# Performance work log

Hardware: AMD Instinct MI355X
Metric: run time of the kernel (lower is better)

The kernel has to match this reference:

```python
import jax, jax.numpy as jnp
import numpy as np

H, P, G, NS, K = 8, 64, 64, 64, 3          # heads, dim_head, slice_num, d_state, d_conv
D_INNER = H * P                            # 512
CONV_DIM = D_INNER + 2 * NS                # 640
D_IN_PROJ = 2 * D_INNER + 2 * NS + 2 * H   # 1168


def setup_inputs() -> dict:
    key = jax.random.key(0)
    ks = jax.random.split(key, 10)
    dim, Bsz, N = 256, 4, 8192
    s = 0.02
    return {
        "x": jax.random.normal(ks[0], (Bsz, N, dim), jnp.float32),
        "W_fx": jax.random.normal(ks[1], (D_INNER, dim), jnp.float32) * s,
        "b_fx": jnp.zeros((D_INNER,), jnp.float32),
        "W_x": jax.random.normal(ks[2], (D_INNER, dim), jnp.float32) * s,
        "b_x": jnp.zeros((D_INNER,), jnp.float32),
        "W_slice": jax.random.normal(ks[3], (G, P), jnp.float32) * s,
        "b_slice": jnp.zeros((G,), jnp.float32),
        "temperature": jnp.full((1, H, 1, 1), 0.5, jnp.float32),
        "hy_in_w": jax.random.normal(ks[4], (D_IN_PROJ, D_INNER), jnp.float32) * s,
        "hy_conv_w": jax.random.normal(ks[5], (CONV_DIM, K), jnp.float32) * s,
        "hy_conv_b": jnp.zeros((CONV_DIM,), jnp.float32),
        "hy_dt_bias": jnp.log(jnp.expm1(jnp.full((H,), 0.01, jnp.float32))),
        "hy_A_log": jnp.log(jnp.linspace(1.0, 16.0, H)).astype(jnp.float32),
        "hy_D": jnp.ones((H,), jnp.float32),
        "hy_fcD_w": jax.random.normal(ks[6], (H, D_INNER), jnp.float32) * s,
        "hy_norm_w": jnp.ones((D_INNER,), jnp.float32),
        "hy_out_w": jax.random.normal(ks[7], (D_INNER, D_INNER), jnp.float32) * s,
        "out_w": jax.random.normal(ks[8], (dim, D_INNER), jnp.float32) * s,
        "out_b": jnp.zeros((dim,), jnp.float32),
    }


def _hydra(u, in_w, conv_w, conv_b, dt_bias, A_log, Dp, fcD_w, norm_w, out_w):
    # Bidirectional Mamba2-style selective scan (Hydra, non mem-eff path).
    Bt, L, _ = u.shape
    zxbcdt = u @ in_w.T                                   # (B, L, 1168)
    z = zxbcdt[..., :D_INNER]
    xBC = zxbcdt[..., D_INNER:D_INNER + CONV_DIM]
    dt = zxbcdt[..., -2 * H:]
    # fwd dts for fwd copies, time-flipped bwd dts stacked along batch
    dt = jnp.concatenate([dt[..., :H], jnp.flip(dt[..., H:], axis=1)], axis=0)
    dt = jax.nn.softplus(dt + dt_bias)                    # (2B, L, H)
    # depthwise causal conv, kernel K, left pad K-1 then silu
    xp = jnp.pad(xBC, ((0, 0), (K - 1, 0), (0, 0)))
    xBC = sum(xp[:, k:k + L, :] * conv_w[:, k] for k in range(K)) + conv_b
    xBC = jax.nn.silu(xBC)
    x = xBC[..., :D_INNER]
    Bm = xBC[..., D_INNER:D_INNER + NS]
    Cm = xBC[..., D_INNER + NS:]
    x_og = x
    x2 = jnp.concatenate([x, jnp.flip(x, 1)], 0).reshape(2 * Bt, L, H, P)
    B2 = jnp.concatenate([Bm, jnp.flip(Bm, 1)], 0)        # (2B, L, NS)
    C2 = jnp.concatenate([Cm, jnp.flip(Cm, 1)], 0)
    dA = jnp.exp(dt * (-jnp.exp(A_log)))                  # (2B, L, H)
    dBx = jnp.einsum('blh,bln,blhp->blhpn', dt, B2, x2)   # (2B, L, H, P, NS)

    def step(h, inp):
        dA_t, dBx_t, C_t = inp
        h = h * dA_t[:, :, None, None] + dBx_t
        return h, jnp.einsum('bhpn,bn->bhp', h, C_t)

    h0 = jnp.zeros((2 * Bt, H, P, NS), u.dtype)
    _, ys = jax.lax.scan(step, h0, (dA.transpose(1, 0, 2), dBx.transpose(1, 0, 2, 3, 4), C2.transpose(1, 0, 2)))
    y = ys.transpose(1, 0, 2, 3).reshape(2 * Bt, L, D_INNER)
    y_fw, y_bw = y[:Bt], jnp.flip(y[Bt:], 1)
    # quasiseparable: strictly-lower (shift fwd) + strictly-upper (shift bwd) + diagonal
    y = jnp.pad(y_fw[:, :-1], ((0, 0), (1, 0), (0, 0))) + jnp.pad(y_bw[:, 1:], ((0, 0), (0, 1), (0, 0)))
    y = y + x_og * jnp.repeat(x_og @ fcD_w.T + Dp, P, axis=-1)
    # gated RMSNorm (gate before norm), then out projection
    yg = y * jax.nn.silu(z)
    yg = yg * jax.lax.rsqrt(jnp.mean(jnp.square(yg), -1, keepdims=True) + 1e-5) * norm_w
    return yg @ out_w.T


def reference(x, W_fx, b_fx, W_x, b_x, W_slice, b_slice, temperature,
              hy_in_w, hy_conv_w, hy_conv_b, hy_dt_bias, hy_A_log, hy_D,
              hy_fcD_w, hy_norm_w, hy_out_w, out_w, out_b):
    B, N, _ = x.shape
    fx = (x @ W_fx.T + b_fx).reshape(B, N, H, P).transpose(0, 2, 1, 3)   # (B,H,N,P)
    xm = (x @ W_x.T + b_x).reshape(B, N, H, P).transpose(0, 2, 1, 3)
    temp = jnp.maximum(temperature, 1e-6)
    sw = jax.nn.softmax((xm @ W_slice.T + b_slice) / temp, axis=-1)      # (B,H,N,G)
    snorm = sw.sum(2)                                                     # (B,H,G)
    st = jnp.einsum('bhnc,bhng->bhgc', fx, sw) / (snorm + 1e-5)[..., None]
    st = st.transpose(0, 2, 1, 3).reshape(B, G, D_INNER)                  # (B,G,512)
    ot = _hydra(st, hy_in_w, hy_conv_w, hy_conv_b, hy_dt_bias, hy_A_log, hy_D,
                hy_fcD_w, hy_norm_w, hy_out_w)
    ot = ot.reshape(B, G, H, P).transpose(0, 2, 1, 3)                     # (B,H,G,P)
    out = jnp.einsum('bhgc,bhng->bhnc', ot, sw).transpose(0, 2, 1, 3).reshape(B, N, D_INNER)
    return out @ out_w.T + out_b
```

## Files before the change

kernel.cpp:

```cpp
#include <hip/hip_runtime.h>
#include <hip/hip_bf16.h>
#include <cstdint>
#include <cstddef>

#define Hh 8
#define DIN 512
#define CONVD 640
#define DPROJ 1168
#define NTOK 8192
#define DIM 256

typedef __attribute__((ext_vector_type(8))) short short8;
typedef __attribute__((ext_vector_type(4))) float f32x4;

static __device__ __forceinline__ float sigmoidf_(float x) { return 1.f / (1.f + expf(-x)); }
static __device__ __forceinline__ unsigned short f2b(float f) {
  __hip_bfloat16 h = __float2bfloat16(f);
  return *(unsigned short*)&h;
}
static __device__ __forceinline__ float b2f(unsigned short u) {
  union { unsigned int i; float f; } cv; cv.i = ((unsigned int)u) << 16; return cv.f;
}

__global__ __launch_bounds__(256) void k_cvt(
    const float* __restrict__ x, const float* __restrict__ wfx, const float* __restrict__ wx,
    const float* __restrict__ outw, const float* __restrict__ inw, const float* __restrict__ how,
    const float* __restrict__ bfx, const float* __restrict__ bx,
    unsigned short* __restrict__ xb, unsigned short* __restrict__ wcat,
    unsigned short* __restrict__ outwb, unsigned short* __restrict__ inwb,
    unsigned short* __restrict__ howb, float* __restrict__ bcat) {
  const int e = (blockIdx.x * 256 + threadIdx.x) * 4;
  if (e >= 9641984) {
    const int i = e - 9641984;
    float4 v;
    if (i < 512) v = *(const float4*)(bfx + i);
    else         v = *(const float4*)(bx + (i - 512));
    *(float4*)(bcat + i) = v;
    return;
  }
  const float* src; unsigned short* dst; int i;
  if (e < 8388608)       { i = e;           src = x;    dst = xb; }
  else if (e < 8519680)  { i = e - 8388608; src = wfx;  dst = wcat; }
  else if (e < 8650752)  { i = e - 8519680; src = wx;   dst = wcat + 131072; }
  else if (e < 8781824)  { i = e - 8650752; src = outw; dst = outwb; }
  else if (e < 9379840)  { i = e - 8781824; src = inw;  dst = inwb; }
  else                   { i = e - 9379840; src = how;  dst = howb; }
  float4 v = *(const float4*)(src + i);
  ushort4 o;
  o.x = f2b(v.x); o.y = f2b(v.y); o.z = f2b(v.z); o.w = f2b(v.w);
  *(ushort4*)(dst + i) = o;
}

__global__ __launch_bounds__(256) void k_fxxm(
    const unsigned short* __restrict__ xb, const unsigned short* __restrict__ wcat,
    const float* __restrict__ bcat, unsigned short* __restrict__ cb) {
  __shared__ unsigned short lds[17408];
  unsigned short* As = lds;
  unsigned short* Bs = lds + 8320;
  const int tid = threadIdx.x;
  const int m0 = blockIdx.x * 128;
  const int n0 = blockIdx.y * 128;
  const int w = tid >> 6, lane = tid & 63;
  const int l15 = lane & 15, kq = lane >> 4;
  const int wm = (w & 1) * 64, wn = (w >> 1) * 64;
  float bs[4];
#pragma unroll
  for (int j = 0; j < 4; ++j) bs[j] = bcat[n0 + wn + j * 16 + l15];
  f32x4 acc[4][4];
#pragma unroll
  for (int i = 0; i < 4; ++i)
#pragma unroll
    for (int j = 0; j < 4; ++j) acc[i][j] = (f32x4){0.f, 0.f, 0.f, 0.f};
  for (int kt = 0; kt < 256; kt += 64) {
#pragma unroll
    for (int i = 0; i < 4; ++i) {
      const int c = tid + 256 * i, m = c >> 3, kb = c & 7;
      *(short8*)&As[(kb * 130 + m) * 8] = *(const short8*)&xb[(size_t)(m0 + m) * 256 + kt + kb * 8];
      *(short8*)&Bs[(kb * 130 + m) * 8] = *(const short8*)&wcat[(size_t)(n0 + m) * 256 + kt + kb * 8];
    }
    __syncthreads();
#pragma unroll
    for (int kw = 0; kw < 2; ++kw) {
      short8 af[4], bfr[4];
#pragma unroll
      for (int i = 0; i < 4; ++i) {
        af[i]  = *(const short8*)&As[((kw * 4 + kq) * 130 + wm + i * 16 + l15) * 8];
        bfr[i] = *(const short8*)&Bs[((kw * 4 + kq) * 130 + wn + i * 16 + l15) * 8];
      }
#pragma unroll
      for (int i = 0; i < 4; ++i)
#pragma unroll
        for (int j = 0; j < 4; ++j)
          acc[i][j] = __builtin_amdgcn_mfma_f32_16x16x32_bf16(af[i], bfr[j], acc[i][j], 0, 0, 0);
    }
    __syncthreads();
  }
  unsigned short* Cs = lds;
#pragma unroll
  for (int i = 0; i < 4; ++i)
#pragma unroll
    for (int j = 0; j < 4; ++j)
#pragma unroll
      for (int r = 0; r < 4; ++r) {
        const int m = wm + i * 16 + kq * 4 + r;
        const int n = wn + j * 16 + l15;
        Cs[m * 136 + n] = f2b(acc[i][j][r] + bs[j]);
      }
  __syncthreads();
#pragma unroll
  for (int it = 0; it < 8; ++it) {
    const int c = tid + 256 * it;
    const int m = c >> 4, seg = c & 15;
    *(short8*)&cb[(size_t)(m0 + m) * 1024 + n0 + seg * 8] = *(const short8*)&Cs[m * 136 + seg * 8];
  }
}

__global__ __launch_bounds__(256) void k_sw(
    const unsigned short* __restrict__ cb, const float* __restrict__ Wslice,
    const float* __restrict__ bslice, const float* __restrict__ temperature,
    unsigned short* __restrict__ swb) {
  __shared__ unsigned short s_sw[256][72];
  const int tid = threadIdx.x;
  const int bh = blockIdx.y;
  const int b = bh >> 3, h = bh & 7;
  const int n0 = blockIdx.x * 256;
  const int w = tid >> 6, lane = tid & 63;
  const int l15 = lane & 15, kq = lane >> 4;
  const float invt = 1.f / fmaxf(temperature[h], 1e-6f);
  short8 bfr[2][4];
#pragma unroll
  for (int kt = 0; kt < 2; ++kt)
#pragma unroll
    for (int j = 0; j < 4; ++j) {
      const float* wp = Wslice + (j * 16 + l15) * 64 + kt * 32 + kq * 8;
      short8 t;
#pragma unroll
      for (int u = 0; u < 8; ++u) t[u] = (short)f2b(wp[u]);
      bfr[kt][j] = t;
    }
  float bs[4];
#pragma unroll
  for (int j = 0; j < 4; ++j) bs[j] = bslice[j * 16 + l15];
  f32x4 acc[4][4];
#pragma unroll
  for (int i = 0; i < 4; ++i)
#pragma unroll
    for (int j = 0; j < 4; ++j) acc[i][j] = (f32x4){0.f, 0.f, 0.f, 0.f};
#pragma unroll
  for (int kt = 0; kt < 2; ++kt) {
    short8 af[4];
#pragma unroll
    for (int i = 0; i < 4; ++i)
      af[i] = *(const short8*)&cb[((size_t)(b * NTOK) + n0 + w * 64 + i * 16 + l15) * 1024 +
                                  512 + h * 64 + kt * 32 + kq * 8];
#pragma unroll
    for (int i = 0; i < 4; ++i)
#pragma unroll
      for (int j = 0; j < 4; ++j)
        acc[i][j] = __builtin_amdgcn_mfma_f32_16x16x32_bf16(af[i], bfr[kt][j], acc[i][j], 0, 0, 0);
  }
#pragma unroll
  for (int i = 0; i < 4; ++i)
#pragma unroll
    for (int r = 0; r < 4; ++r) {
      float v[4];
      float m = -1e30f;
#pragma unroll
      for (int j = 0; j < 4; ++j) { v[j] = (acc[i][j][r] + bs[j]) * invt; m = fmaxf(m, v[j]); }
#pragma unroll
      for (int off = 8; off; off >>= 1) m = fmaxf(m, __shfl_xor(m, off));
      float s = 0.f;
#pragma unroll
      for (int j = 0; j < 4; ++j) { v[j] = expf(v[j] - m); s += v[j]; }
#pragma unroll
      for (int off = 8; off; off >>= 1) s += __shfl_xor(s, off);
      const float inv = 1.f / s;
      const int row = w * 64 + i * 16 + kq * 4 + r;
#pragma unroll
      for (int j = 0; j < 4; ++j) s_sw[row][j * 16 + l15] = f2b(v[j] * inv);
    }
  __syncthreads();
#pragma unroll
  for (int it = 0; it < 8; ++it) {
    const int c = tid + 256 * it;
    const int row = c >> 3, seg = c & 7;
    *(short8*)&swb[((size_t)bh * NTOK + n0 + row) * 64 + seg * 8] =
        *(const short8*)&s_sw[row][seg * 8];
  }
}

__global__ __launch_bounds__(256) void k_st(
    const unsigned short* __restrict__ swb, const unsigned short* __restrict__ cb,
    float* __restrict__ st_raw, float* __restrict__ snorm) {
  __shared__ unsigned short swT[64][136];
  __shared__ unsigned short fxT[64][136];
  const int tid = threadIdx.x;
  const int bh = blockIdx.y;
  const int b = bh >> 3, h = bh & 7;
  const int nbase = blockIdx.x * 512;
  const int w = tid >> 6, lane = tid & 63;
  const int l15 = lane & 15, kq = lane >> 4;
  f32x4 acc[4];
#pragma unroll
  for (int i = 0; i < 4; ++i) acc[i] = (f32x4){0.f, 0.f, 0.f, 0.f};
  float sn = 0.f;
  for (int nc = 0; nc < 4; ++nc) {
    const int n0 = nbase + nc * 128;
#pragma unroll
    for (int i = 0; i < 4; ++i) {
      const int c = tid + 256 * i, n = c >> 3, gc = c & 7;
      short8 sv = *(const short8*)&swb[((size_t)bh * NTOK + n0 + n) * 64 + gc * 8];
      short8 fv = *(const short8*)&cb[((size_t)(b * NTOK) + n0 + n) * 1024 + h * 64 + gc * 8];
#pragma unroll
      for (int u = 0; u < 8; ++u) {
        swT[gc * 8 + u][n] = (unsigned short)sv[u];
        fxT[gc * 8 + u][n] = (unsigned short)fv[u];
      }
    }
    __syncthreads();
    {
      const int g = tid & 63, q = tid >> 6;
#pragma unroll
      for (int nn = 0; nn < 32; ++nn) sn += b2f(swT[g][q * 32 + nn]);
    }
#pragma unroll
    for (int kw = 0; kw < 4; ++kw) {
      short8 bfr = *(const short8*)&fxT[w * 16 + l15][kw * 32 + kq * 8];
#pragma unroll
      for (int mi = 0; mi < 4; ++mi) {
        short8 af = *(const short8*)&swT[mi * 16 + l15][kw * 32 + kq * 8];
        acc[mi] = __builtin_amdgcn_mfma_f32_16x16x32_bf16(af, bfr, acc[mi], 0, 0, 0);
      }
    }
    __syncthreads();
  }
  float* stp = st_raw + (size_t)bh * 4096;
#pragma unroll
  for (int mi = 0; mi < 4; ++mi)
#pragma unroll
    for (int r = 0; r < 4; ++r)
      atomicAdd(&stp[(mi * 16 + kq * 4 + r) * 64 + w * 16 + l15], acc[mi][r]);
  atomicAdd(&snorm[bh * 64 + (tid & 63)], sn);
}

__global__ __launch_bounds__(256) void k_stnorm(
    const float* __restrict__ st_raw, const float* __restrict__ snorm,
    unsigned short* __restrict__ st2b) {
  const int idx = blockIdx.x * 256 + threadIdx.x;
  const int p = idx & 63, g = (idx >> 6) & 63, h = (idx >> 12) & 7, b = idx >> 15;
  const float v = st_raw[idx] / (snorm[(b * Hh + h) * 64 + g] + 1e-5f);
  st2b[(size_t)(b * 64 + g) * DIN + h * 64 + p] = f2b(v);
}

__global__ __launch_bounds__(256) void k_inproj(
    const unsigned short* __restrict__ st2b, const unsigned short* __restrict__ inwb,
    float* __restrict__ zx) {
  const int tid = threadIdx.x;
  const int m0 = blockIdx.x * 64;
  const int n0 = blockIdx.y * 64;
  const int w = tid >> 6, lane = tid & 63;
  const int l15 = lane & 15, kq = lane >> 4;
  f32x4 acc[4];
#pragma unroll
  for (int j = 0; j < 4; ++j) acc[j] = (f32x4){0.f, 0.f, 0.f, 0.f};
  const int arow = m0 + w * 16 + l15;
#pragma unroll
  for (int kc = 0; kc < 16; ++kc) {
    const short8 af = *(const short8*)&st2b[(size_t)arow * DIN + kc * 32 + kq * 8];
#pragma unroll
    for (int j = 0; j < 4; ++j) {
      int brow = n0 + j * 16 + l15;
      if (brow >= DPROJ) brow = 0;
      const short8 bfr = *(const short8*)&inwb[(size_t)brow * DIN + kc * 32 + kq * 8];
      acc[j] = __builtin_amdgcn_mfma_f32_16x16x32_bf16(af, bfr, acc[j], 0, 0, 0);
    }
  }
#pragma unroll
  for (int j = 0; j < 4; ++j)
#pragma unroll
    for (int r = 0; r < 4; ++r) {
      const int m = m0 + w * 16 + kq * 4 + r;
      const int c = n0 + j * 16 + l15;
      if (c < DPROJ) zx[(size_t)m * DPROJ + c] = acc[j][r];
    }
}

__global__ __launch_bounds__(256) void k_prep(
    const float* __restrict__ zx, const float* __restrict__ convw, const float* __restrict__ convb,
    const float* __restrict__ dtbias, const float* __restrict__ Alog,
    float* __restrict__ xbc, float* __restrict__ dt2, float* __restrict__ ldA2) {
  const int idx = blockIdx.x * 256 + threadIdx.x;
  const int NCONV = 4 * 64 * CONVD;
  if (idx < NCONV) {
    const int c = idx % CONVD;
    const int l = (idx / CONVD) & 63;
    const int b = idx / (CONVD * 64);
    float acc = convb[c];
#pragma unroll
    for (int k = 0; k < 3; ++k) {
      const int ls = l - 2 + k;
      if (ls >= 0) acc += zx[(size_t)(b * 64 + ls) * DPROJ + DIN + c] * convw[c * 3 + k];
    }
    xbc[idx] = acc * sigmoidf_(acc);
  } else if (idx < NCONV + 8 * 64 * 8) {
    const int j = idx - NCONV;
    const int h = j & 7, l = (j >> 3) & 63, bb = j >> 9;
    float raw;
    if (bb < 4) raw = zx[(size_t)(bb * 64 + l) * DPROJ + 1152 + h];
    else        raw = zx[(size_t)((bb - 4) * 64 + (63 - l)) * DPROJ + 1160 + h];
    const float d = raw + dtbias[h];
    const float sp = (d > 20.f) ? d : log1pf(expf(d));
    dt2[j] = sp;
    ldA2[j] = sp * -expf(Alog[h]);
  }
}

__global__ __launch_bounds__(256) void k_ssm(
    const float* __restrict__ xbc, const float* __restrict__ dt2, const float* __restrict__ ldA2,
    float* __restrict__ ys) {
  __shared__ unsigned short s_C[64][72];
  __shared__ unsigned short s_Bm[64][72];
  __shared__ unsigned short s_X[64][72];
  __shared__ unsigned short s_G[64][72];
  __shared__ float s_L[64];
  __shared__ float s_dt[64];
  const int blk = blockIdx.x;
  const int h = blk & 7, bb = blk >> 3;
  const int b = (bb < 4) ? bb : bb - 4;
  const bool rev = bb >= 4;
  const int tid = threadIdx.x;
  const int w = tid >> 6, lane = tid & 63;
  const int l15 = lane & 15, kq = lane >> 4;
  {
    const int l = tid >> 2, part = tid & 3;
    const int t = rev ? 63 - l : l;
    const float* src = xbc + (size_t)(b * 64 + l) * CONVD + DIN + part * 32;
#pragma unroll
    for (int u = 0; u < 32; u += 4) {
      float4 v = *(const float4*)(src + u);
      const int c = part * 32 + u;
      unsigned short* dst = (c < 64) ? &s_Bm[t][c] : &s_C[t][c - 64];
      dst[0] = f2b(v.x); dst[1] = f2b(v.y); dst[2] = f2b(v.z); dst[3] = f2b(v.w);
    }
    const float* xs = xbc + (size_t)(b * 64 + l) * CONVD + h * 64 + part * 16;
#pragma unroll
    for (int u = 0; u < 16; u += 4) {
      float4 v = *(const float4*)(xs + u);
      const int p = part * 16 + u;
      s_X[p + 0][t] = f2b(v.x); s_X[p + 1][t] = f2b(v.y);
      s_X[p + 2][t] = f2b(v.z); s_X[p + 3][t] = f2b(v.w);
    }
  }
  if (w == 0) {
    const float dtv = dt2[(bb * 64 + lane) * 8 + h];
    float ld = ldA2[(bb * 64 + lane) * 8 + h];
#pragma unroll
    for (int off = 1; off < 64; off <<= 1) {
      const float o = __shfl_up(ld, off);
      if (lane >= off) ld += o;
    }
    s_L[lane] = ld;
    s_dt[lane] = dtv;
  }
  __syncthreads();
  f32x4 accS[4];
#pragma unroll
  for (int i = 0; i < 4; ++i) accS[i] = (f32x4){0.f, 0.f, 0.f, 0.f};
#pragma unroll
  for (int kw = 0; kw < 2; ++kw) {
    const short8 bfr = *(const short8*)&s_Bm[w * 16 + l15][kw * 32 + kq * 8];
#pragma unroll
    for (int i = 0; i < 4; ++i) {
      const short8 af = *(const short8*)&s_C[i * 16 + l15][kw * 32 + kq * 8];
      accS[i] = __builtin_amdgcn_mfma_f32_16x16x32_bf16(af, bfr, accS[i], 0, 0, 0);
    }
  }
  const int s_idx = w * 16 + l15;
  const float Ls = s_L[s_idx];
  const float dts = s_dt[s_idx];
#pragma unroll
  for (int i = 0; i < 4; ++i)
#pragma unroll
    for (int r = 0; r < 4; ++r) {
      const int t = i * 16 + kq * 4 + r;
      const float g = (s_idx <= t) ? accS[i][r] * expf(s_L[t] - Ls) * dts : 0.f;
      s_G[t][s_idx] = f2b(g);
    }
  __syncthreads();
  f32x4 accY[4];
#pragma unroll
  for (int i = 0; i < 4; ++i) accY[i] = (f32x4){0.f, 0.f, 0.f, 0.f};
#pragma unroll
  for (int kw = 0; kw < 2; ++kw) {
    const short8 bfr = *(const short8*)&s_X[w * 16 + l15][kw * 32 + kq * 8];
#pragma unroll
    for (int i = 0; i < 4; ++i) {
      const short8 af = *(const short8*)&s_G[i * 16 + l15][kw * 32 + kq * 8];
      accY[i] = __builtin_amdgcn_mfma_f32_16x16x32_bf16(af, bfr, accY[i], 0, 0, 0);
    }
  }
#pragma unroll
  for (int i = 0; i < 4; ++i)
#pragma unroll
    for (int r = 0; r < 4; ++r) {
      const int t = i * 16 + kq * 4 + r;
      ys[(((size_t)(bb * 64 + t) * 8 + h) << 6) + w * 16 + l15] = accY[i][r];
    }
}

__global__ __launch_bounds__(256) void k_gate(
    const float* __restrict__ ys, const float* __restrict__ xbc, const float* __restrict__ zx,
    const float* __restrict__ fcdw, const float* __restrict__ Dp,
    const float* __restrict__ normw, unsigned short* __restrict__ ygb) {
  __shared__ float red[256][9];
  __shared__ float s_xfc[8];
  const int bl = blockIdx.x;
  const int b = bl >> 6, l = bl & 63;
  const int tid = threadIdx.x;
  const float xog0 = xbc[(size_t)bl * CONVD + tid];
  const float xog1 = xbc[(size_t)bl * CONVD + 256 + tid];
#pragma unroll
  for (int h = 0; h < 8; ++h)
    red[tid][h] = xog0 * fcdw[h * DIN + tid] + xog1 * fcdw[h * DIN + 256 + tid];
  __syncthreads();
  for (int s = 128; s > 0; s >>= 1) {
    if (tid < s) {
#pragma unroll
      for (int h = 0; h < 8; ++h) red[tid][h] += red[tid + s][h];
    }
    __syncthreads();
  }
  if (tid < 8) s_xfc[tid] = red[0][tid] + Dp[tid];
  __syncthreads();
  float ygv[2];
  float sumsq = 0.f;
#pragma unroll
  for (int ci = 0; ci < 2; ++ci) {
    const int c = tid + ci * 256;
    const int h = c >> 6, p = c & 63;
    float yv = 0.f;
    if (l >= 1)  yv += ys[(((size_t)(b * 64 + (l - 1)) * 8 + h) << 6) + p];
    if (l <= 62) yv += ys[(((size_t)((4 + b) * 64 + (62 - l)) * 8 + h) << 6) + p];
    const float xog = (ci == 0) ? xog0 : xog1;
    yv += xog * s_xfc[h];
    const float z = zx[(size_t)bl * DPROJ + c];
    const float g = yv * (z * sigmoidf_(z));
    ygv[ci] = g;
    sumsq += g * g;
  }
  red[tid][0] = sumsq;
  __syncthreads();
  for (int s = 128; s > 0; s >>= 1) {
    if (tid < s) red[tid][0] += red[tid + s][0];
    __syncthreads();
  }
  const float scale = 1.f / sqrtf(red[0][0] / 512.f + 1e-5f);
#pragma unroll
  for (int ci = 0; ci < 2; ++ci) {
    const int c = tid + ci * 256;
    ygb[(size_t)bl * DIN + c] = f2b(ygv[ci] * scale * normw[c]);
  }
}

__global__ __launch_bounds__(256) void k_oproj(
    const unsigned short* __restrict__ ygb, const unsigned short* __restrict__ howb,
    unsigned short* __restrict__ otT) {
  __shared__ unsigned short Cs[64][72];
  const int tid = threadIdx.x;
  const int b = blockIdx.x;
  const int h = blockIdx.y;
  const int m0 = b * 64, n0 = h * 64;
  const int w = tid >> 6, lane = tid & 63;
  const int l15 = lane & 15, kq = lane >> 4;
  f32x4 acc[4];
#pragma unroll
  for (int j = 0; j < 4; ++j) acc[j] = (f32x4){0.f, 0.f, 0.f, 0.f};
  const int arow = m0 + w * 16 + l15;
#pragma unroll
  for (int kc = 0; kc < 16; ++kc) {
    const short8 af = *(const short8*)&ygb[(size_t)arow * DIN + kc * 32 + kq * 8];
#pragma unroll
    for (int j = 0; j < 4; ++j) {
      const int brow = n0 + j * 16 + l15;
      const short8 bfr = *(const short8*)&howb[(size_t)brow * DIN + kc * 32 + kq * 8];
      acc[j] = __builtin_amdgcn_mfma_f32_16x16x32_bf16(af, bfr, acc[j], 0, 0, 0);
    }
  }
#pragma unroll
  for (int j = 0; j < 4; ++j)
#pragma unroll
    for (int r = 0; r < 4; ++r) {
      const int g = w * 16 + kq * 4 + r;
      const int p = j * 16 + l15;
      Cs[p][g] = f2b(acc[j][r]);
    }
  __syncthreads();
#pragma unroll
  for (int it = 0; it < 2; ++it) {
    const int c = tid + 256 * it;
    const int p = c >> 3, seg = c & 7;
    *(short8*)&otT[(((size_t)(b * 8 + h) * 64 + p) << 6) + seg * 8] = *(const short8*)&Cs[p][seg * 8];
  }
}

__global__ __launch_bounds__(256) void k_mix(
    const unsigned short* __restrict__ swb, const unsigned short* __restrict__ otT,
    unsigned short* __restrict__ interb) {
  __shared__ unsigned short lds[20736];
  unsigned short* As = lds;
  unsigned short* Bs = lds + 16512;
  const int tid = threadIdx.x;
  const int bh = blockIdx.y;
  const int b = bh >> 3, h = bh & 7;
  const int n0 = blockIdx.x * 256;
  const int w = tid >> 6, lane = tid & 63;
  const int l15 = lane & 15, kq = lane >> 4;
#pragma unroll
  for (int i = 0; i < 8; ++i) {
    const int c = tid + 256 * i, m = c >> 3, kb = c & 7;
    *(short8*)&As[(kb * 258 + m) * 8] = *(const short8*)&swb[((size_t)bh * NTOK + n0 + m) * 64 + kb * 8];
  }
#pragma unroll
  for (int i = 0; i < 2; ++i) {
    const int c = tid + 256 * i, p = c >> 3, kb = c & 7;
    *(short8*)&Bs[(kb * 66 + p) * 8] = *(const short8*)&otT[((size_t)bh * 64 + p) * 64 + kb * 8];
  }
  __syncthreads();
  f32x4 acc[4][4];
#pragma unroll
  for (int i = 0; i < 4; ++i)
#pragma unroll
    for (int j = 0; j < 4; ++j) acc[i][j] = (f32x4){0.f, 0.f, 0.f, 0.f};
#pragma unroll
  for (int kw = 0; kw < 2; ++kw) {
    short8 af[4], bfr[4];
#pragma unroll
    for (int i = 0; i < 4; ++i) {
      af[i]  = *(const short8*)&As[((kw * 4 + kq) * 258 + w * 64 + i * 16 + l15) * 8];
      bfr[i] = *(const short8*)&Bs[((kw * 4 + kq) * 66 + i * 16 + l15) * 8];
    }
#pragma unroll
    for (int i = 0; i < 4; ++i)
#pragma unroll
      for (int j = 0; j < 4; ++j)
        acc[i][j] = __builtin_amdgcn_mfma_f32_16x16x32_bf16(af[i], bfr[j], acc[i][j], 0, 0, 0);
  }
  __syncthreads();
  unsigned short* Cs = lds;
#pragma unroll
  for (int i = 0; i < 4; ++i)
#pragma unroll
    for (int j = 0; j < 4; ++j)
#pragma unroll
      for (int r = 0; r < 4; ++r) {
        const int m = w * 64 + i * 16 + kq * 4 + r;
        const int n = j * 16 + l15;
        Cs[m * 72 + n] = f2b(acc[i][j][r]);
      }
  __syncthreads();
#pragma unroll
  for (int it = 0; it < 8; ++it) {
    const int c = tid + 256 * it;
    const int row = c >> 3, seg = c & 7;
    *(short8*)&interb[((size_t)(b * NTOK) + n0 + row) * 512 + h * 64 + seg * 8] =
        *(const short8*)&Cs[row * 72 + seg * 8];
  }
}

__global__ __launch_bounds__(256) void k_final(
    const unsigned short* __restrict__ interb, const unsigned short* __restrict__ outwb,
    const float* __restrict__ outb, float* __restrict__ out) {
  __shared__ float ldsf[8448];
  unsigned short* ls = (unsigned short*)ldsf;
  unsigned short* As = ls;
  unsigned short* Bs = ls + 8320;
  const int tid = threadIdx.x;
  const int m0 = blockIdx.x * 128;
  const int n0 = blockIdx.y * 128;
  const int w = tid >> 6, lane = tid & 63;
  const int l15 = lane & 15, kq = lane >> 4;
  const int wm = (w & 1) * 64, wn = (w >> 1) * 64;
  float ob[4];
#pragma unroll
  for (int j = 0; j < 4; ++j) ob[j] = outb[n0 + wn + j * 16 + l15];
  f32x4 acc[4][4];
#pragma unroll
  for (int i = 0; i < 4; ++i)
#pragma unroll
    for (int j = 0; j < 4; ++j) acc[i][j] = (f32x4){0.f, 0.f, 0.f, 0.f};
  for (int kt = 0; kt < DIN; kt += 64) {
#pragma unroll
    for (int i = 0; i < 4; ++i) {
      const int c = tid + 256 * i, m = c >> 3, kb = c & 7;
      *(short8*)&As[(kb * 130 + m) * 8] = *(const short8*)&interb[(size_t)(m0 + m) * DIN + kt + kb * 8];
      *(short8*)&Bs[(kb * 130 + m) * 8] = *(const short8*)&outwb[(size_t)(n0 + m) * DIN + kt + kb * 8];
    }
    __syncthreads();
#pragma unroll
    for (int kw = 0; kw < 2; ++kw) {
      short8 af[4], bfr[4];
#pragma unroll
      for (int i = 0; i < 4; ++i) {
        af[i]  = *(const short8*)&As[((kw * 4 + kq) * 130 + wm + i * 16 + l15) * 8];
        bfr[i] = *(const short8*)&Bs[((kw * 4 + kq) * 130 + wn + i * 16 + l15) * 8];
      }
#pragma unroll
      for (int i = 0; i < 4; ++i)
#pragma unroll
        for (int j = 0; j < 4; ++j)
          acc[i][j] = __builtin_amdgcn_mfma_f32_16x16x32_bf16(af[i], bfr[j], acc[i][j], 0, 0, 0);
    }
    __syncthreads();
  }
  float* Cs = ldsf;
#pragma unroll
  for (int pass = 0; pass < 2; ++pass) {
    __syncthreads();
    if ((w & 1) == pass) {
#pragma unroll
      for (int i = 0; i < 4; ++i)
#pragma unroll
        for (int j = 0; j < 4; ++j)
#pragma unroll
          for (int r = 0; r < 4; ++r) {
            const int ml = i * 16 + kq * 4 + r;
            const int n = wn + j * 16 + l15;
            Cs[ml * 132 + n] = acc[i][j][r] + ob[j];
          }
    }
    __syncthreads();
#pragma unroll
    for (int it = 0; it < 8; ++it) {
      const int c = tid + 256 * it;
      const int m = c >> 5, seg = c & 31;
      *(float4*)&out[(size_t)(m0 + pass * 64 + m) * 256 + n0 + seg * 4] =
          *(const float4*)&Cs[m * 132 + seg * 4];
    }
  }
}

extern "C" void kernel_launch(void* const* d_in, const int* in_sizes, int n_in,
                              void* d_out, int out_size, void* d_ws, size_t ws_size,
                              hipStream_t stream) {
  const float* x      = (const float*)d_in[0];
  const float* Wfx    = (const float*)d_in[1];
  const float* bfx    = (const float*)d_in[2];
  const float* Wx     = (const float*)d_in[3];
  const float* bx     = (const float*)d_in[4];
  const float* Wslice = (const float*)d_in[5];
  const float* bslice = (const float*)d_in[6];
  const float* temp   = (const float*)d_in[7];
  const float* inw    = (const float*)d_in[8];
  const float* convw  = (const float*)d_in[9];
  const float* convb  = (const float*)d_in[10];
  const float* dtbias = (const float*)d_in[11];
  const float* Alog   = (const float*)d_in[12];
  const float* Dp     = (const float*)d_in[13];
  const float* fcdw   = (const float*)d_in[14];
  const float* normw  = (const float*)d_in[15];
  const float* how    = (const float*)d_in[16];
  const float* outw   = (const float*)d_in[17];
  const float* outb   = (const float*)d_in[18];

  unsigned short* us = (unsigned short*)d_ws;
  unsigned short* cb     = us;
  unsigned short* swb    = cb + 33554432;
  unsigned short* interb = swb + 16777216;
  unsigned short* xbfb   = interb + 16777216;
  unsigned short* wcatb  = xbfb + 8388608;
  unsigned short* outwbf = wcatb + 262144;
  unsigned short* otTb   = outwbf + 131072;
  unsigned short* inwb   = otTb + 131072;
  unsigned short* howb   = inwb + 598016;
  unsigned short* st2b   = howb + 262144;
  unsigned short* ygbb   = st2b + 131072;
  float* fbase = (float*)(ygbb + 131072);
  float* bcat   = fbase;
  float* st_raw = bcat + 1024;
  float* snorm  = st_raw + 131072;
  float* zx     = snorm + 2048;
  float* xbc    = zx + 299008;
  float* dt2    = xbc + 163840;
  float* ldA2   = dt2 + 4096;
  float* ysb    = ldA2 + 4096;

  hipMemsetAsync(st_raw, 0, (131072 + 2048) * sizeof(float), stream);

  k_cvt   <<<dim3(9417),     256, 0, stream>>>(x, Wfx, Wx, outw, inw, how, bfx, bx,
                                               xbfb, wcatb, outwbf, inwb, howb, bcat);
  k_fxxm  <<<dim3(256, 8),   256, 0, stream>>>(xbfb, wcatb, bcat, cb);
  k_sw    <<<dim3(32, 32),   256, 0, stream>>>(cb, Wslice, bslice, temp, swb);
  k_st    <<<dim3(16, 32),   256, 0, stream>>>(swb, cb, st_raw, snorm);
  k_stnorm<<<dim3(512),      256, 0, stream>>>(st_raw, snorm, st2b);
  k_inproj<<<dim3(4, 19),    256, 0, stream>>>(st2b, inwb, zx);
  k_prep  <<<dim3(656),      256, 0, stream>>>(zx, convw, convb, dtbias, Alog, xbc, dt2, ldA2);
  k_ssm   <<<dim3(64),       256, 0, stream>>>(xbc, dt2, ldA2, ysb);
  k_gate  <<<dim3(256),      256, 0, stream>>>(ysb, xbc, zx, fcdw, Dp, normw, ygbb);
  k_oproj <<<dim3(4, 8),     256, 0, stream>>>(ygbb, howb, otTb);
  k_mix   <<<dim3(32, 32),   256, 0, stream>>>(swb, otTb, interb);
  k_final <<<dim3(256, 2),   256, 0, stream>>>(interb, outwbf, outb, (float*)d_out);
}
```

Measured before the change: 278.8 us.

## Fuse x conversion into projection GEMM, slice softmax into front, mix with final

Three fusions cut DRAM round trips of large intermediates. The x fp32-to-bf16 conversion moves into the fx/xm GEMM load path. The slice-weight softmax is computed in the same kernel from the xm tile in LDS, so the xm half of cb is never written. The mix and output projection are merged into one kernel that keeps the per-token 512-wide intermediate in LDS instead of writing interb. The trade-offs are more work per block, higher LDS use in k_mixfinal (about 66KB), and direct global-memory operand loads in the mix stage.

After: 267.7 us. -4.0%, faster.

```diff
diff --git a/kernel.cpp b/kernel.cpp
--- a/kernel.cpp
+++ b/kernel.cpp
@@ -23,15 +23,15 @@
 }
 
 __global__ __launch_bounds__(256) void k_cvt(
-    const float* __restrict__ x, const float* __restrict__ wfx, const float* __restrict__ wx,
-    const float* __restrict__ outw, const float* __restrict__ inw, const float* __restrict__ how,
+    const float* __restrict__ wfx, const float* __restrict__ wx, const float* __restrict__ outw,
+    const float* __restrict__ inw, const float* __restrict__ how,
     const float* __restrict__ bfx, const float* __restrict__ bx,
-    unsigned short* __restrict__ xb, unsigned short* __restrict__ wcat,
-    unsigned short* __restrict__ outwb, unsigned short* __restrict__ inwb,
-    unsigned short* __restrict__ howb, float* __restrict__ bcat) {
+    unsigned short* __restrict__ wcat, unsigned short* __restrict__ outwb,
+    unsigned short* __restrict__ inwb, unsigned short* __restrict__ howb,
+    float* __restrict__ bcat) {
   const int e = (blockIdx.x * 256 + threadIdx.x) * 4;
-  if (e >= 9641984) {
-    const int i = e - 9641984;
+  if (e >= 1253376) {
+    const int i = e - 1253376;
     float4 v;
     if (i < 512) v = *(const float4*)(bfx + i);
     else         v = *(const float4*)(bx + (i - 512));
@@ -39,21 +39,22 @@
     return;
   }
   const float* src; unsigned short* dst; int i;
-  if (e < 8388608)       { i = e;           src = x;    dst = xb; }
-  else if (e < 8519680)  { i = e - 8388608; src = wfx;  dst = wcat; }
-  else if (e < 8650752)  { i = e - 8519680; src = wx;   dst = wcat + 131072; }
-  else if (e < 8781824)  { i = e - 8650752; src = outw; dst = outwb; }
-  else if (e < 9379840)  { i = e - 8781824; src = inw;  dst = inwb; }
-  else                   { i = e - 9379840; src = how;  dst = howb; }
+  if (e < 131072)        { i = e;           src = wfx;  dst = wcat; }
+  else if (e < 262144)   { i = e - 131072;  src = wx;   dst = wcat + 131072; }
+  else if (e < 393216)   { i = e - 262144;  src = outw; dst = outwb; }
+  else if (e < 991232)   { i = e - 393216;  src = inw;  dst = inwb; }
+  else                   { i = e - 991232;  src = how;  dst = howb; }
   float4 v = *(const float4*)(src + i);
   ushort4 o;
   o.x = f2b(v.x); o.y = f2b(v.y); o.z = f2b(v.z); o.w = f2b(v.w);
   *(ushort4*)(dst + i) = o;
 }
 
-__global__ __launch_bounds__(256) void k_fxxm(
-    const unsigned short* __restrict__ xb, const unsigned short* __restrict__ wcat,
-    const float* __restrict__ bcat, unsigned short* __restrict__ cb) {
+__global__ __launch_bounds__(256) void k_front(
+    const float* __restrict__ x, const unsigned short* __restrict__ wcat,
+    const float* __restrict__ bcat, const float* __restrict__ Wslice,
+    const float* __restrict__ bslice, const float* __restrict__ temperature,
+    unsigned short* __restrict__ cb, unsigned short* __restrict__ swb) {
   __shared__ unsigned short lds[17408];
   unsigned short* As = lds;
   unsigned short* Bs = lds + 8320;
@@ -75,7 +76,15 @@
 #pragma unroll
     for (int i = 0; i < 4; ++i) {
       const int c = tid + 256 * i, m = c >> 3, kb = c & 7;
-      *(short8*)&As[(kb * 130 + m) * 8] = *(const short8*)&xb[(size_t)(m0 + m) * 256 + kt + kb * 8];
+      const float* xs = &x[(size_t)(m0 + m) * 256 + kt + kb * 8];
+      float4 v0 = *(const float4*)xs;
+      float4 v1 = *(const float4*)(xs + 4);
+      short8 av;
+      av[0] = (short)f2b(v0.x); av[1] = (short)f2b(v0.y);
+      av[2] = (short)f2b(v0.z); av[3] = (short)f2b(v0.w);
+      av[4] = (short)f2b(v1.x); av[5] = (short)f2b(v1.y);
+      av[6] = (short)f2b(v1.z); av[7] = (short)f2b(v1.w);
+      *(short8*)&As[(kb * 130 + m) * 8] = av;
       *(short8*)&Bs[(kb * 130 + m) * 8] = *(const short8*)&wcat[(size_t)(n0 + m) * 256 + kt + kb * 8];
     }
     __syncthreads();
@@ -107,27 +116,18 @@
         Cs[m * 136 + n] = f2b(acc[i][j][r] + bs[j]);
       }
   __syncthreads();
-#pragma unroll
-  for (int it = 0; it < 8; ++it) {
-    const int c = tid + 256 * it;
-    const int m = c >> 4, seg = c & 15;
-    *(short8*)&cb[(size_t)(m0 + m) * 1024 + n0 + seg * 8] = *(const short8*)&Cs[m * 136 + seg * 8];
-  }
-}
-
-__global__ __launch_bounds__(256) void k_sw(
-    const unsigned short* __restrict__ cb, const float* __restrict__ Wslice,
-    const float* __restrict__ bslice, const float* __restrict__ temperature,
-    unsigned short* __restrict__ swb) {
-  __shared__ unsigned short s_sw[256][72];
-  const int tid = threadIdx.x;
-  const int bh = blockIdx.y;
-  const int b = bh >> 3, h = bh & 7;
-  const int n0 = blockIdx.x * 256;
-  const int w = tid >> 6, lane = tid & 63;
-  const int l15 = lane & 15, kq = lane >> 4;
-  const float invt = 1.f / fmaxf(temperature[h], 1e-6f);
-  short8 bfr[2][4];
+  if (blockIdx.y < 4) {
+#pragma unroll
+    for (int it = 0; it < 8; ++it) {
+      const int c = tid + 256 * it;
+      const int m = c >> 4, seg = c & 15;
+      *(short8*)&cb[(size_t)(m0 + m) * 512 + n0 + seg * 8] = *(const short8*)&Cs[m * 136 + seg * 8];
+    }
+    return;
+  }
+  const int h0 = (n0 - 512) >> 6;
+  const int bidx = m0 >> 13, nb = m0 & (NTOK - 1);
+  short8 sbfr[2][4];
 #pragma unroll
   for (int kt = 0; kt < 2; ++kt)
 #pragma unroll
@@ -136,56 +136,64 @@
       short8 t;
 #pragma unroll
       for (int u = 0; u < 8; ++u) t[u] = (short)f2b(wp[u]);
-      bfr[kt][j] = t;
-    }
-  float bs[4];
-#pragma unroll
-  for (int j = 0; j < 4; ++j) bs[j] = bslice[j * 16 + l15];
-  f32x4 acc[4][4];
-#pragma unroll
-  for (int i = 0; i < 4; ++i)
-#pragma unroll
-    for (int j = 0; j < 4; ++j) acc[i][j] = (f32x4){0.f, 0.f, 0.f, 0.f};
-#pragma unroll
-  for (int kt = 0; kt < 2; ++kt) {
-    short8 af[4];
-#pragma unroll
-    for (int i = 0; i < 4; ++i)
-      af[i] = *(const short8*)&cb[((size_t)(b * NTOK) + n0 + w * 64 + i * 16 + l15) * 1024 +
-                                  512 + h * 64 + kt * 32 + kq * 8];
-#pragma unroll
-    for (int i = 0; i < 4; ++i)
-#pragma unroll
-      for (int j = 0; j < 4; ++j)
-        acc[i][j] = __builtin_amdgcn_mfma_f32_16x16x32_bf16(af[i], bfr[kt][j], acc[i][j], 0, 0, 0);
-  }
-#pragma unroll
-  for (int i = 0; i < 4; ++i)
-#pragma unroll
-    for (int r = 0; r < 4; ++r) {
-      float v[4];
-      float m = -1e30f;
-#pragma unroll
-      for (int j = 0; j < 4; ++j) { v[j] = (acc[i][j][r] + bs[j]) * invt; m = fmaxf(m, v[j]); }
-#pragma unroll
-      for (int off = 8; off; off >>= 1) m = fmaxf(m, __shfl_xor(m, off));
-      float s = 0.f;
-#pragma unroll
-      for (int j = 0; j < 4; ++j) { v[j] = expf(v[j] - m); s += v[j]; }
-#pragma unroll
-      for (int off = 8; off; off >>= 1) s += __shfl_xor(s, off);
-      const float inv = 1.f / s;
-      const int row = w * 64 + i * 16 + kq * 4 + r;
-#pragma unroll
-      for (int j = 0; j < 4; ++j) s_sw[row][j * 16 + l15] = f2b(v[j] * inv);
-    }
+      sbfr[kt][j] = t;
+    }
+  float sbs[4];
+#pragma unroll
+  for (int j = 0; j < 4; ++j) sbs[j] = bslice[j * 16 + l15];
+  f32x4 sacc[2][2][4];
+#pragma unroll
+  for (int hl = 0; hl < 2; ++hl)
+#pragma unroll
+    for (int i = 0; i < 2; ++i)
+#pragma unroll
+      for (int j = 0; j < 4; ++j) sacc[hl][i][j] = (f32x4){0.f, 0.f, 0.f, 0.f};
+#pragma unroll
+  for (int hl = 0; hl < 2; ++hl)
+#pragma unroll
+    for (int kt = 0; kt < 2; ++kt) {
+      short8 af[2];
+#pragma unroll
+      for (int i = 0; i < 2; ++i)
+        af[i] = *(const short8*)&Cs[(w * 32 + i * 16 + l15) * 136 + hl * 64 + kt * 32 + kq * 8];
+#pragma unroll
+      for (int i = 0; i < 2; ++i)
+#pragma unroll
+        for (int j = 0; j < 4; ++j)
+          sacc[hl][i][j] = __builtin_amdgcn_mfma_f32_16x16x32_bf16(af[i], sbfr[kt][j], sacc[hl][i][j], 0, 0, 0);
+    }
+  __syncthreads();
+#pragma unroll
+  for (int hl = 0; hl < 2; ++hl) {
+    const float invt = 1.f / fmaxf(temperature[h0 + hl], 1e-6f);
+#pragma unroll
+    for (int i = 0; i < 2; ++i)
+#pragma unroll
+      for (int r = 0; r < 4; ++r) {
+        float v[4];
+        float m = -1e30f;
+#pragma unroll
+        for (int j = 0; j < 4; ++j) { v[j] = (sacc[hl][i][j][r] + sbs[j]) * invt; m = fmaxf(m, v[j]); }
+#pragma unroll
+        for (int off = 8; off; off >>= 1) m = fmaxf(m, __shfl_xor(m, off));
+        float s = 0.f;
+#pragma unroll
+        for (int j = 0; j < 4; ++j) { v[j] = expf(v[j] - m); s += v[j]; }
+#pragma unroll
+        for (int off = 8; off; off >>= 1) s += __shfl_xor(s, off);
+        const float inv = 1.f / s;
+        const int row = w * 32 + i * 16 + kq * 4 + r;
+#pragma unroll
+        for (int j = 0; j < 4; ++j) Cs[row * 136 + hl * 64 + j * 16 + l15] = f2b(v[j] * inv);
+      }
+  }
   __syncthreads();
 #pragma unroll
   for (int it = 0; it < 8; ++it) {
     const int c = tid + 256 * it;
-    const int row = c >> 3, seg = c & 7;
-    *(short8*)&swb[((size_t)bh * NTOK + n0 + row) * 64 + seg * 8] =
-        *(const short8*)&s_sw[row][seg * 8];
+    const int head = c >> 10, row = (c >> 3) & 127, seg = c & 7;
+    *(short8*)&swb[((size_t)(bidx * 8 + h0 + head) * NTOK + nb + row) * 64 + seg * 8] =
+        *(const short8*)&Cs[row * 136 + head * 64 + seg * 8];
   }
 }
 
@@ -210,7 +218,7 @@
     for (int i = 0; i < 4; ++i) {
       const int c = tid + 256 * i, n = c >> 3, gc = c & 7;
       short8 sv = *(const short8*)&swb[((size_t)bh * NTOK + n0 + n) * 64 + gc * 8];
-      short8 fv = *(const short8*)&cb[((size_t)(b * NTOK) + n0 + n) * 1024 + h * 64 + gc * 8];
+      short8 fv = *(const short8*)&cb[((size_t)(b * NTOK) + n0 + n) * 512 + h * 64 + gc * 8];
 #pragma unroll
       for (int u = 0; u < 8; ++u) {
         swT[gc * 8 + u][n] = (unsigned short)sv[u];
@@ -503,106 +511,33 @@
   }
 }
 
-__global__ __launch_bounds__(256) void k_mix(
+__global__ __launch_bounds__(256) void k_mixfinal(
     const unsigned short* __restrict__ swb, const unsigned short* __restrict__ otT,
-    unsigned short* __restrict__ interb) {
-  __shared__ unsigned short lds[20736];
-  unsigned short* As = lds;
-  unsigned short* Bs = lds + 16512;
+    const unsigned short* __restrict__ outwb, const float* __restrict__ outb,
+    float* __restrict__ out) {
+  __shared__ unsigned short lm[33280];
+  const int blk = blockIdx.x;
+  const int b = blk >> 7;
+  const int t0 = (blk & 127) * 64;
   const int tid = threadIdx.x;
-  const int bh = blockIdx.y;
-  const int b = bh >> 3, h = bh & 7;
-  const int n0 = blockIdx.x * 256;
   const int w = tid >> 6, lane = tid & 63;
   const int l15 = lane & 15, kq = lane >> 4;
 #pragma unroll
-  for (int i = 0; i < 8; ++i) {
-    const int c = tid + 256 * i, m = c >> 3, kb = c & 7;
-    *(short8*)&As[(kb * 258 + m) * 8] = *(const short8*)&swb[((size_t)bh * NTOK + n0 + m) * 64 + kb * 8];
-  }
-#pragma unroll
-  for (int i = 0; i < 2; ++i) {
-    const int c = tid + 256 * i, p = c >> 3, kb = c & 7;
-    *(short8*)&Bs[(kb * 66 + p) * 8] = *(const short8*)&otT[((size_t)bh * 64 + p) * 64 + kb * 8];
-  }
-  __syncthreads();
-  f32x4 acc[4][4];
-#pragma unroll
-  for (int i = 0; i < 4; ++i)
-#pragma unroll
-    for (int j = 0; j < 4; ++j) acc[i][j] = (f32x4){0.f, 0.f, 0.f, 0.f};
-#pragma unroll
-  for (int kw = 0; kw < 2; ++kw) {
-    short8 af[4], bfr[4];
-#pragma unroll
-    for (int i = 0; i < 4; ++i) {
-      af[i]  = *(const short8*)&As[((kw * 4 + kq) * 258 + w * 64 + i * 16 + l15) * 8];
-      bfr[i] = *(const short8*)&Bs[((kw * 4 + kq) * 66 + i * 16 + l15) * 8];
-    }
+  for (int hh = 0; hh < 2; ++hh) {
+    const int h = w * 2 + hh;
+    const int bh = b * 8 + h;
+    f32x4 acc[4][4];
 #pragma unroll
     for (int i = 0; i < 4; ++i)
 #pragma unroll
-      for (int j = 0; j < 4; ++j)
-        acc[i][j] = __builtin_amdgcn_mfma_f32_16x16x32_bf16(af[i], bfr[j], acc[i][j], 0, 0, 0);
-  }
-  __syncthreads();
-  unsigned short* Cs = lds;
-#pragma unroll
-  for (int i = 0; i < 4; ++i)
-#pragma unroll
-    for (int j = 0; j < 4; ++j)
-#pragma unroll
-      for (int r = 0; r < 4; ++r) {
-        const int m = w * 64 + i * 16 + kq * 4 + r;
-        const int n = j * 16 + l15;
-        Cs[m * 72 + n] = f2b(acc[i][j][r]);
-      }
-  __syncthreads();
-#pragma unroll
-  for (int it = 0; it < 8; ++it) {
-    const int c = tid + 256 * it;
-    const int row = c >> 3, seg = c & 7;
-    *(short8*)&interb[((size_t)(b * NTOK) + n0 + row) * 512 + h * 64 + seg * 8] =
-        *(const short8*)&Cs[row * 72 + seg * 8];
-  }
-}
-
-__global__ __launch_bounds__(256) void k_final(
-    const unsigned short* __restrict__ interb, const unsigned short* __restrict__ outwb,
-    const float* __restrict__ outb, float* __restrict__ out) {
-  __shared__ float ldsf[8448];
-  unsigned short* ls = (unsigned short*)ldsf;
-  unsigned short* As = ls;
-  unsigned short* Bs = ls + 8320;
-  const int tid = threadIdx.x;
-  const int m0 = blockIdx.x * 128;
-  const int n0 = blockIdx.y * 128;
-  const int w = tid >> 6, lane = tid & 63;
-  const int l15 = lane & 15, kq = lane >> 4;
-  const int wm = (w & 1) * 64, wn = (w >> 1) * 64;
-  float ob[4];
-#pragma unroll
-  for (int j = 0; j < 4; ++j) ob[j] = outb[n0 + wn + j * 16 + l15];
-  f32x4 acc[4][4];
-#pragma unroll
-  for (int i = 0; i < 4; ++i)
-#pragma unroll
-    for (int j = 0; j < 4; ++j) acc[i][j] = (f32x4){0.f, 0.f, 0.f, 0.f};
-  for (int kt = 0; kt < DIN; kt += 64) {
-#pragma unroll
-    for (int i = 0; i < 4; ++i) {
-      const int c = tid + 256 * i, m = c >> 3, kb = c & 7;
-      *(short8*)&As[(kb * 130 + m) * 8] = *(const short8*)&interb[(size_t)(m0 + m) * DIN + kt + kb * 8];
-      *(short8*)&Bs[(kb * 130 + m) * 8] = *(const short8*)&outwb[(size_t)(n0 + m) * DIN + kt + kb * 8];
-    }
-    __syncthreads();
-#pragma unroll
-    for (int kw = 0; kw < 2; ++kw) {
+      for (int j = 0; j < 4; ++j) acc[i][j] = (f32x4){0.f, 0.f, 0.f, 0.f};
+#pragma unroll
+    for (int kt = 0; kt < 2; ++kt) {
       short8 af[4], bfr[4];
 #pragma unroll
       for (int i = 0; i < 4; ++i) {
-        af[i]  = *(const short8*)&As[((kw * 4 + kq) * 130 + wm + i * 16 + l15) * 8];
-        bfr[i] = *(const short8*)&Bs[((kw * 4 + kq) * 130 + wn + i * 16 + l15) * 8];
+        af[i]  = *(const short8*)&swb[((size_t)bh * NTOK + t0 + i * 16 + l15) * 64 + kt * 32 + kq * 8];
+        bfr[i] = *(const short8*)&otT[(((size_t)bh * 64 + i * 16 + l15) << 6) + kt * 32 + kq * 8];
       }
 #pragma unroll
       for (int i = 0; i < 4; ++i)
@@ -610,32 +545,53 @@
         for (int j = 0; j < 4; ++j)
           acc[i][j] = __builtin_amdgcn_mfma_f32_16x16x32_bf16(af[i], bfr[j], acc[i][j], 0, 0, 0);
     }
-    __syncthreads();
-  }
-  float* Cs = ldsf;
-#pragma unroll
-  for (int pass = 0; pass < 2; ++pass) {
-    __syncthreads();
-    if ((w & 1) == pass) {
-#pragma unroll
-      for (int i = 0; i < 4; ++i)
-#pragma unroll
-        for (int j = 0; j < 4; ++j)
-#pragma unroll
-          for (int r = 0; r < 4; ++r) {
-            const int ml = i * 16 + kq * 4 + r;
-            const int n = wn + j * 16 + l15;
-            Cs[ml * 132 + n] = acc[i][j][r] + ob[j];
-          }
-    }
-    __syncthreads();
-#pragma unroll
-    for (int it = 0; it < 8; ++it) {
-      const int c = tid + 256 * it;
-      const int m = c >> 5, seg = c & 31;
-      *(float4*)&out[(size_t)(m0 + pass * 64 + m) * 256 + n0 + seg * 4] =
-          *(const float4*)&Cs[m * 132 + seg * 4];
-    }
+#pragma unroll
+    for (int i = 0; i < 4; ++i)
+#pragma unroll
+      for (int j = 0; j < 4; ++j)
+#pragma unroll
+        for (int r = 0; r < 4; ++r)
+          lm[(i * 16 + kq * 4 + r) * 520 + h * 64 + j * 16 + l15] = f2b(acc[i][j][r]);
+  }
+  __syncthreads();
+  float ob[4];
+#pragma unroll
+  for (int j = 0; j < 4; ++j) ob[j] = outb[w * 64 + j * 16 + l15];
+  f32x4 facc[4][4];
+#pragma unroll
+  for (int i = 0; i < 4; ++i)
+#pragma unroll
+    for (int j = 0; j < 4; ++j) facc[i][j] = (f32x4){0.f, 0.f, 0.f, 0.f};
+#pragma unroll
+  for (int kt = 0; kt < 16; ++kt) {
+    short8 af[4], bfr[4];
+#pragma unroll
+    for (int i = 0; i < 4; ++i) {
+      af[i]  = *(const short8*)&lm[(i * 16 + l15) * 520 + kt * 32 + kq * 8];
+      bfr[i] = *(const short8*)&outwb[(size_t)(w * 64 + i * 16 + l15) * 512 + kt * 32 + kq * 8];
+    }
+#pragma unroll
+    for (int i = 0; i < 4; ++i)
+#pragma unroll
+      for (int j = 0; j < 4; ++j)
+        facc[i][j] = __builtin_amdgcn_mfma_f32_16x16x32_bf16(af[i], bfr[j], facc[i][j], 0, 0, 0);
+  }
+  __syncthreads();
+  float* lf = (float*)lm;
+#pragma unroll
+  for (int i = 0; i < 4; ++i)
+#pragma unroll
+    for (int j = 0; j < 4; ++j)
+#pragma unroll
+      for (int r = 0; r < 4; ++r)
+        lf[(i * 16 + kq * 4 + r) * 260 + w * 64 + j * 16 + l15] = facc[i][j][r] + ob[j];
+  __syncthreads();
+#pragma unroll
+  for (int it = 0; it < 16; ++it) {
+    const int c = tid + 256 * it;
+    const int row = c >> 6, seg = c & 63;
+    *(float4*)&out[((size_t)(b * NTOK + t0 + row)) * 256 + seg * 4] =
+        *(const float4*)&lf[row * 260 + seg * 4];
   }
 }
 
@@ -664,10 +620,8 @@
 
   unsigned short* us = (unsigned short*)d_ws;
   unsigned short* cb     = us;
-  unsigned short* swb    = cb + 33554432;
-  unsigned short* interb = swb + 16777216;
-  unsigned short* xbfb   = interb + 16777216;
-  unsigned short* wcatb  = xbfb + 8388608;
+  unsigned short* swb    = cb + 16777216;
+  unsigned short* wcatb  = swb + 16777216;
   unsigned short* outwbf = wcatb + 262144;
   unsigned short* otTb   = outwbf + 131072;
   unsigned short* inwb   = otTb + 131072;
@@ -686,17 +640,15 @@
 
   hipMemsetAsync(st_raw, 0, (131072 + 2048) * sizeof(float), stream);
 
-  k_cvt   <<<dim3(9417),     256, 0, stream>>>(x, Wfx, Wx, outw, inw, how, bfx, bx,
-                                               xbfb, wcatb, outwbf, inwb, howb, bcat);
-  k_fxxm  <<<dim3(256, 8),   256, 0, stream>>>(xbfb, wcatb, bcat, cb);
-  k_sw    <<<dim3(32, 32),   256, 0, stream>>>(cb, Wslice, bslice, temp, swb);
-  k_st    <<<dim3(16, 32),   256, 0, stream>>>(swb, cb, st_raw, snorm);
-  k_stnorm<<<dim3(512),      256, 0, stream>>>(st_raw, snorm, st2b);
-  k_inproj<<<dim3(4, 19),    256, 0, stream>>>(st2b, inwb, zx);
-  k_prep  <<<dim3(656),      256, 0, stream>>>(zx, convw, convb, dtbias, Alog, xbc, dt2, ldA2);
-  k_ssm   <<<dim3(64),       256, 0, stream>>>(xbc, dt2, ldA2, ysb);
-  k_gate  <<<dim3(256),      256, 0, stream>>>(ysb, xbc, zx, fcdw, Dp, normw, ygbb);
-  k_oproj <<<dim3(4, 8),     256, 0, stream>>>(ygbb, howb, otTb);
-  k_mix   <<<dim3(32, 32),   256, 0, stream>>>(swb, otTb, interb);
-  k_final <<<dim3(256, 2),   256, 0, stream>>>(interb, outwbf, outb, (float*)d_out);
-}
+  k_cvt     <<<dim3(1225),    256, 0, stream>>>(Wfx, Wx, outw, inw, how, bfx, bx,
+                                                wcatb, outwbf, inwb, howb, bcat);
+  k_front   <<<dim3(256, 8),  256, 0, stream>>>(x, wcatb, bcat, Wslice, bslice, temp, cb, swb);
+  k_st      <<<dim3(16, 32),  256, 0, stream>>>(swb, cb, st_raw, snorm);
+  k_stnorm  <<<dim3(512),     256, 0, stream>>>(st_raw, snorm, st2b);
+  k_inproj  <<<dim3(4, 19),   256, 0, stream>>>(st2b, inwb, zx);
+  k_prep    <<<dim3(656),     256, 0, stream>>>(zx, convw, convb, dtbias, Alog, xbc, dt2, ldA2);
+  k_ssm     <<<dim3(64),      256, 0, stream>>>(xbc, dt2, ldA2, ysb);
+  k_gate    <<<dim3(256),     256, 0, stream>>>(ysb, xbc, zx, fcdw, Dp, normw, ygbb);
+  k_oproj   <<<dim3(4, 8),    256, 0, stream>>>(ygbb, howb, otTb);
+  k_mixfinal<<<dim3(512),     256, 0, stream>>>(swb, otTb, outwbf, outb, (float*)d_out);
+}
```
